# Kernel tuning notes

Measured on AMD Instinct MI355X. Metric: run time of the kernel, lower is better.

## Reference

```python
import jax, jax.numpy as jnp
import numpy as np

B, C, Ci, T, H, W = 8, 1024, 512, 8, 16, 16
BN_EPS = 1e-5


def setup_inputs() -> dict:
    key = jax.random.key(0)
    ks = jax.random.split(key, 13)
    s = 1.0 / np.sqrt(C)
    si = 1.0 / np.sqrt(Ci)
    return {
        "x": jax.random.normal(ks[0], (B, C, T, H, W), jnp.float32),
        "g_w": jax.random.normal(ks[1], (Ci, C), jnp.float32) * s,
        "g_b": jax.random.normal(ks[2], (Ci,), jnp.float32) * 0.01,
        "theta_w": jax.random.normal(ks[3], (Ci, C), jnp.float32) * s,
        "theta_b": jax.random.normal(ks[4], (Ci,), jnp.float32) * 0.01,
        "phi_w": jax.random.normal(ks[5], (Ci, C), jnp.float32) * s,
        "phi_b": jax.random.normal(ks[6], (Ci,), jnp.float32) * 0.01,
        "W_w": jax.random.normal(ks[7], (C, Ci), jnp.float32) * si,
        "W_b": jax.random.normal(ks[8], (C,), jnp.float32) * 0.01,
        "bn_gamma": jax.random.normal(ks[9], (C,), jnp.float32),
        "bn_beta": jax.random.normal(ks[10], (C,), jnp.float32) * 0.1,
        "bn_mean": jax.random.normal(ks[11], (C,), jnp.float32) * 0.1,
        "bn_var": jax.random.uniform(ks[12], (C,), jnp.float32) + 0.5,
    }


def reference(x, g_w, g_b, theta_w, theta_b, phi_w, phi_b, W_w, W_b,
              bn_gamma, bn_beta, bn_mean, bn_var):
    b = x.shape[0]
    xf = x.reshape(b, x.shape[1], -1)  # (B, C, N), N = T*H*W

    def proj(w, bias):  # 1x1 conv over flattened spatial dims == channel GEMM
        return jnp.einsum('oc,bcn->bon', w, xf) + bias[None, :, None]

    g_x = proj(g_w, g_b).transpose(0, 2, 1)          # (B, N, Ci)
    theta_x = proj(theta_w, theta_b).transpose(0, 2, 1)  # (B, N, Ci)
    phi_x = proj(phi_w, phi_b)                        # (B, Ci, N)

    f = jnp.einsum('bnc,bcm->bnm', theta_x, phi_x)    # (B, N, N) full scores
    f_div_C = jax.nn.softmax(f, axis=-1)
    y = jnp.einsum('bnm,bmc->bnc', f_div_C, g_x)      # (B, N, Ci)
    y = y.transpose(0, 2, 1)                          # (B, Ci, N)

    W_y = jnp.einsum('oc,bcn->bon', W_w, y) + W_b[None, :, None]
    # BatchNorm (inference mode with running stats)
    inv = jax.lax.rsqrt(bn_var + BN_EPS)
    W_y = (W_y - bn_mean[None, :, None]) * (inv * bn_gamma)[None, :, None] + bn_beta[None, :, None]

    z = W_y + xf
    return z.reshape(x.shape)
```

## Files before the change

kernel.cpp:

```cpp
#include <hip/hip_runtime.h>


#define B_  8
#define C_  1024
#define CI_ 512
#define N_  2048

typedef _Float16 half_t;
typedef __attribute__((ext_vector_type(8))) _Float16 f16x8;
typedef __attribute__((ext_vector_type(4))) _Float16 f16x4;
typedef __attribute__((ext_vector_type(4))) float     f32x4;

__device__ __forceinline__ void gload16(const void* g, void* l) {
  __builtin_amdgcn_global_load_lds(
      (__attribute__((address_space(1))) unsigned int*)(g),
      (__attribute__((address_space(3))) unsigned int*)(l),
      16, 0, 0);
}

__device__ __forceinline__ void gemm128(const half_t* Ag, long lda,
                                        const half_t* Bg, long ldb,
                                        int K,
                                        half_t* lA, half_t* lB,
                                        f32x4 acc[4][4])
{
  const int tid  = threadIdx.x;
  const int lane = tid & 63;
  const int wid  = tid >> 6;
  const int wm   = wid >> 1, wn = wid & 1;
  const int frow = lane & 15;
  const int g4   = lane >> 4;

  for (int k0 = 0; k0 < K; k0 += 64) {
#pragma unroll
    for (int it = 0; it < 4; ++it) {
      int c = it * 256 + tid;
      int row = c >> 3, slot = (c & 7) ^ (row & 7);
      gload16(Ag + (long)row * lda + (k0 + slot * 8), (char*)lA + c * 16);
    }
#pragma unroll
    for (int it = 0; it < 4; ++it) {
      int c = it * 256 + tid;
      int row = c >> 3, slot = (c & 7) ^ (row & 7);
      gload16(Bg + (long)row * ldb + (k0 + slot * 8), (char*)lB + c * 16);
    }
    __syncthreads();
#pragma unroll
    for (int kk = 0; kk < 2; ++kk) {
      f16x8 af[4], bfr[4];
#pragma unroll
      for (int i = 0; i < 4; ++i) {
        int row  = wm * 64 + i * 16 + frow;
        int slot = (kk * 4 + g4) ^ (row & 7);
        af[i] = *(const f16x8*)(lA + row * 64 + slot * 8);
      }
#pragma unroll
      for (int j = 0; j < 4; ++j) {
        int row  = wn * 64 + j * 16 + frow;
        int slot = (kk * 4 + g4) ^ (row & 7);
        bfr[j] = *(const f16x8*)(lB + row * 64 + slot * 8);
      }
#pragma unroll
      for (int i = 0; i < 4; ++i)
#pragma unroll
        for (int j = 0; j < 4; ++j)
          acc[i][j] = __builtin_amdgcn_mfma_f32_16x16x32_f16(af[i], bfr[j], acc[i][j], 0, 0, 0);
    }
    __syncthreads();
  }
}

__device__ __forceinline__ void zero_acc(f32x4 acc[4][4]) {
  f32x4 z = {0.f, 0.f, 0.f, 0.f};
#pragma unroll
  for (int i = 0; i < 4; ++i)
#pragma unroll
    for (int j = 0; j < 4; ++j) acc[i][j] = z;
}

__device__ __forceinline__ void dump_acc(float* ep, const f32x4 acc[4][4],
                                         int wm, int wn, int lane, int pass,
                                         const float* bias_row)
{
  if (wm != pass) return;
  int r4 = (lane >> 4) * 4, cc = lane & 15;
#pragma unroll
  for (int i = 0; i < 4; ++i) {
#pragma unroll
    for (int r = 0; r < 4; ++r) {
      int row = i * 16 + r4 + r;
      float bv = bias_row ? bias_row[row] : 0.0f;
#pragma unroll
      for (int j = 0; j < 4; ++j)
        ep[row * 128 + wn * 64 + j * 16 + cc] = acc[i][j][r] + bv;
    }
  }
}

__global__ __launch_bounds__(256) void k_prep(
    const float* theta_w, const float* phi_w, const float* g_w,
    const float* W_w, const float* W_b,
    const float* gamma, const float* beta, const float* mean, const float* var,
    half_t* Wcat, half_t* Wfin, float* bnA, float* bnB)
{
  const int PW = CI_ * C_;
  int idx = blockIdx.x * 256 + threadIdx.x;
  if (idx < PW)               Wcat[idx] = (half_t)theta_w[idx];
  else if (idx < 2 * PW)      Wcat[idx] = (half_t)phi_w[idx - PW];
  else if (idx < 3 * PW)      Wcat[idx] = (half_t)g_w[idx - 2 * PW];
  else if (idx < 4 * PW)      Wfin[idx - 3 * PW] = (half_t)W_w[idx - 3 * PW];
  else if (idx < 4 * PW + C_) {
    int o = idx - 4 * PW;
    float sc = gamma[o] * rsqrtf(var[o] + 1e-5f);
    bnA[o] = sc;
    bnB[o] = (W_b[o] - mean[o]) * sc + beta[o];
  }
}

__global__ __launch_bounds__(256) void k_transpose(const float* x, half_t* xT)
{
  __shared__ float t[32][33];
  int b = blockIdx.z, c0 = blockIdx.y * 32, n0 = blockIdx.x * 32;
  int tx = threadIdx.x, ty = threadIdx.y;
  const float* xp = x + ((long)b * C_ + c0) * N_ + n0;
#pragma unroll
  for (int j = 0; j < 4; ++j)
    t[ty + j * 8][tx] = xp[(long)(ty + j * 8) * N_ + tx];
  __syncthreads();
  half_t* xo = xT + ((long)b * N_ + n0) * C_ + c0;
#pragma unroll
  for (int j = 0; j < 4; ++j)
    xo[(long)(ty + j * 8) * C_ + tx] = (half_t)t[tx][ty + j * 8];
}

__global__ __launch_bounds__(256) void k_proj(
    const half_t* Wcat, const half_t* xT,
    const float* theta_b, const float* phi_b, const float* g_b,
    half_t* thetaT, half_t* phiT, half_t* gmat)
{
  __shared__ __align__(16) char smem[32768];
  half_t* lA = (half_t*)smem;
  half_t* lB = (half_t*)(smem + 16384);
  float*  ep = (float*)smem;

  int b = blockIdx.z, m0 = blockIdx.y * 128, n0 = blockIdx.x * 128;
  f32x4 acc[4][4];
  zero_acc(acc);
  gemm128(Wcat + (long)m0 * C_, C_, xT + ((long)b * N_ + n0) * C_, C_, C_, lA, lB, acc);

  int lane = threadIdx.x & 63, wid = threadIdx.x >> 6;
  int wm = wid >> 1, wn = wid & 1;
  int t = threadIdx.x;

  const float* bias = (m0 < 512) ? theta_b : (m0 < 1024) ? phi_b : g_b;
  int m0sub = (m0 < 512) ? m0 : (m0 < 1024) ? m0 - 512 : m0 - 1024;

#pragma unroll
  for (int pass = 0; pass < 2; ++pass) {
    __syncthreads();
    dump_acc(ep, acc, wm, wn, lane, pass, bias + m0sub + pass * 64);
    __syncthreads();
    if (m0 < 1024) {
      half_t* basep = (m0 < 512) ? thetaT : phiT;
      int ncol = t >> 1, ob = (t & 1) * 32;
      half_t* dst = basep + ((long)b * N_ + n0 + ncol) * CI_
                          + (m0sub + pass * 64 + ob);
#pragma unroll
      for (int k2 = 0; k2 < 4; ++k2) {
        f16x8 w;
#pragma unroll
        for (int e = 0; e < 8; ++e)
          w[e] = (half_t)ep[(ob + k2 * 8 + e) * 128 + ncol];
        *(f16x8*)(dst + k2 * 8) = w;
      }
    } else {
#pragma unroll
      for (int k = 0; k < 8; ++k) {
        int lin = t * 4 + k * 1024;
        int row = lin >> 7, col = lin & 127;
        int o = m0sub + pass * 64 + row;
        f32x4 v = *(const f32x4*)(ep + lin);
        f16x4 w = { (half_t)v[0], (half_t)v[1], (half_t)v[2], (half_t)v[3] };
        *(f16x4*)(gmat + ((long)b * CI_ + o) * N_ + n0 + col) = w;
      }
    }
  }
}

__global__ __launch_bounds__(256) void k_qk(
    const half_t* thetaT, const half_t* phiT, float* fbuf, int c0, int rows)
{
  __shared__ __align__(16) char smem[32768];
  half_t* lA = (half_t*)smem;
  half_t* lB = (half_t*)(smem + 16384);
  float*  ep = (float*)smem;

  int b = blockIdx.z, m0 = blockIdx.y * 128, n0 = blockIdx.x * 128;
  f32x4 acc[4][4];
  zero_acc(acc);
  gemm128(thetaT + ((long)b * N_ + c0 + m0) * CI_, CI_,
          phiT   + ((long)b * N_ + n0) * CI_,      CI_, CI_, lA, lB, acc);

  int lane = threadIdx.x & 63, wid = threadIdx.x >> 6;
  int wm = wid >> 1, wn = wid & 1;
  int t = threadIdx.x;
#pragma unroll
  for (int pass = 0; pass < 2; ++pass) {
    __syncthreads();
    dump_acc(ep, acc, wm, wn, lane, pass, nullptr);
    __syncthreads();
#pragma unroll
    for (int k = 0; k < 8; ++k) {
      int lin = t * 4 + k * 1024;
      int row = lin >> 7, col = lin & 127;
      int mr = m0 + pass * 64 + row;
      *(f32x4*)(fbuf + ((long)b * rows + mr) * N_ + n0 + col) =
          *(const f32x4*)(ep + lin);
    }
  }
}

__global__ __launch_bounds__(256) void k_softmax(float* fbuf)
{
  long row = blockIdx.x;
  float* rp = fbuf + row * N_;
  int t = threadIdx.x, lane = t & 63, wid = t >> 6;
  f32x4 a = *(const f32x4*)(rp + t * 8);
  f32x4 c = *(const f32x4*)(rp + t * 8 + 4);
  float m = fmaxf(fmaxf(fmaxf(a[0], a[1]), fmaxf(a[2], a[3])),
                  fmaxf(fmaxf(c[0], c[1]), fmaxf(c[2], c[3])));
#pragma unroll
  for (int o = 1; o < 64; o <<= 1) m = fmaxf(m, __shfl_xor(m, o));
  __shared__ float red[8];
  if (lane == 0) red[wid] = m;
  __syncthreads();
  m = fmaxf(fmaxf(red[0], red[1]), fmaxf(red[2], red[3]));
  float e[8];
  e[0] = __expf(a[0] - m); e[1] = __expf(a[1] - m);
  e[2] = __expf(a[2] - m); e[3] = __expf(a[3] - m);
  e[4] = __expf(c[0] - m); e[5] = __expf(c[1] - m);
  e[6] = __expf(c[2] - m); e[7] = __expf(c[3] - m);
  float s = ((e[0] + e[1]) + (e[2] + e[3])) + ((e[4] + e[5]) + (e[6] + e[7]));
#pragma unroll
  for (int o = 1; o < 64; o <<= 1) s += __shfl_xor(s, o);
  if (lane == 0) red[4 + wid] = s;
  __syncthreads();
  s = (red[4] + red[5]) + (red[6] + red[7]);
  float inv = 1.0f / s;
  f16x8 ph;
#pragma unroll
  for (int k = 0; k < 8; ++k) ph[k] = (half_t)(e[k] * inv);
  *(f16x8*)((half_t*)rp + t * 8) = ph;
}

__global__ __launch_bounds__(256) void k_pv(
    const half_t* P, const half_t* gmat, half_t* ybuf, int c0, int rows)
{
  __shared__ __align__(16) char smem[32768];
  half_t* lA = (half_t*)smem;
  half_t* lB = (half_t*)(smem + 16384);
  float*  ep = (float*)smem;

  int b = blockIdx.z, m0 = blockIdx.y * 128, n0 = blockIdx.x * 128;
  f32x4 acc[4][4];
  zero_acc(acc);
  gemm128(P + ((long)b * rows + m0) * (N_ * 2), N_ * 2,
          gmat + ((long)b * CI_ + n0) * N_,     N_, N_, lA, lB, acc);

  int lane = threadIdx.x & 63, wid = threadIdx.x >> 6;
  int wm = wid >> 1, wn = wid & 1;
  int t = threadIdx.x;
#pragma unroll
  for (int pass = 0; pass < 2; ++pass) {
    __syncthreads();
    dump_acc(ep, acc, wm, wn, lane, pass, nullptr);
    __syncthreads();
#pragma unroll
    for (int k = 0; k < 8; ++k) {
      int lin = t * 4 + k * 1024;
      int row = lin >> 7, col = lin & 127;
      int nr = c0 + m0 + pass * 64 + row;
      f32x4 v = *(const f32x4*)(ep + lin);
      f16x4 w = { (half_t)v[0], (half_t)v[1], (half_t)v[2], (half_t)v[3] };
      *(f16x4*)(ybuf + ((long)b * N_ + nr) * CI_ + n0 + col) = w;
    }
  }
}

__global__ __launch_bounds__(256) void k_final(
    const half_t* Wfin, const half_t* ybuf,
    const float* bnA, const float* bnB, const float* x, float* out)
{
  __shared__ __align__(16) char smem[32768];
  half_t* lA = (half_t*)smem;
  half_t* lB = (half_t*)(smem + 16384);
  float*  ep = (float*)smem;

  int b = blockIdx.z, m0 = blockIdx.y * 128, n0 = blockIdx.x * 128;
  f32x4 acc[4][4];
  zero_acc(acc);
  gemm128(Wfin + (long)m0 * CI_, CI_,
          ybuf + ((long)b * N_ + n0) * CI_, CI_, CI_, lA, lB, acc);

  int lane = threadIdx.x & 63, wid = threadIdx.x >> 6;
  int wm = wid >> 1, wn = wid & 1;
  int t = threadIdx.x;
#pragma unroll
  for (int pass = 0; pass < 2; ++pass) {
    __syncthreads();
    dump_acc(ep, acc, wm, wn, lane, pass, nullptr);
    __syncthreads();
#pragma unroll
    for (int k = 0; k < 8; ++k) {
      int lin = t * 4 + k * 1024;
      int row = lin >> 7, col = lin & 127;
      int o = m0 + pass * 64 + row;
      long idx = ((long)b * C_ + o) * N_ + n0 + col;
      f32x4 v  = *(const f32x4*)(ep + lin);
      f32x4 xi = *(const f32x4*)(x + idx);
      float sA = bnA[o], sB = bnB[o];
      f32x4 w = { v[0] * sA + sB + xi[0], v[1] * sA + sB + xi[1],
                  v[2] * sA + sB + xi[2], v[3] * sA + sB + xi[3] };
      *(f32x4*)(out + idx) = w;
    }
  }
}

extern "C" void kernel_launch(void* const* d_in, const int* in_sizes, int n_in,
                              void* d_out, int out_size, void* d_ws, size_t ws_size,
                              hipStream_t stream)
{
  const float* x       = (const float*)d_in[0];
  const float* g_w     = (const float*)d_in[1];
  const float* g_b     = (const float*)d_in[2];
  const float* theta_w = (const float*)d_in[3];
  const float* theta_b = (const float*)d_in[4];
  const float* phi_w   = (const float*)d_in[5];
  const float* phi_b   = (const float*)d_in[6];
  const float* W_w     = (const float*)d_in[7];
  const float* W_b     = (const float*)d_in[8];
  const float* gamma   = (const float*)d_in[9];
  const float* beta    = (const float*)d_in[10];
  const float* mean    = (const float*)d_in[11];
  const float* var     = (const float*)d_in[12];
  float* out = (float*)d_out;

  char* p = (char*)d_ws;
  auto alloc = [&](size_t bytes) {
    char* r = p; p += (bytes + 255) & ~(size_t)255; return r;
  };
  half_t* xT     = (half_t*)alloc((size_t)B_ * N_ * C_ * 2);
  half_t* Wcat   = (half_t*)alloc((size_t)1536 * C_ * 2);
  half_t* Wfin   = (half_t*)alloc((size_t)C_ * CI_ * 2);
  half_t* thetaT = (half_t*)alloc((size_t)B_ * N_ * CI_ * 2);
  half_t* phiT   = (half_t*)alloc((size_t)B_ * N_ * CI_ * 2);
  half_t* gmat   = (half_t*)alloc((size_t)B_ * CI_ * N_ * 2);
  half_t* ybuf   = (half_t*)alloc((size_t)B_ * N_ * CI_ * 2);
  float*  bnA    = (float*)alloc(C_ * 4);
  float*  bnB    = (float*)alloc(C_ * 4);
  size_t fixed = (size_t)(p - (char*)d_ws);

  int rows;
  if      (fixed + (size_t)B_ * 2048 * N_ * 4 <= ws_size) rows = 2048;
  else if (fixed + (size_t)B_ * 1024 * N_ * 4 <= ws_size) rows = 1024;
  else if (fixed + (size_t)B_ *  512 * N_ * 4 <= ws_size) rows = 512;
  else if (fixed + (size_t)B_ *  256 * N_ * 4 <= ws_size) rows = 256;
  else rows = 128;
  float* fbuf = (float*)alloc((size_t)B_ * rows * N_ * 4);

  k_prep<<<dim3((4 * CI_ * C_ + C_) / 256 + 1), 256, 0, stream>>>(
      theta_w, phi_w, g_w, W_w, W_b, gamma, beta, mean, var, Wcat, Wfin, bnA, bnB);
  k_transpose<<<dim3(N_ / 32, C_ / 32, B_), dim3(32, 8), 0, stream>>>(x, xT);
  k_proj<<<dim3(N_ / 128, 1536 / 128, B_), 256, 0, stream>>>(
      Wcat, xT, theta_b, phi_b, g_b, thetaT, phiT, gmat);
  for (int c0 = 0; c0 < N_; c0 += rows) {
    k_qk<<<dim3(N_ / 128, rows / 128, B_), 256, 0, stream>>>(thetaT, phiT, fbuf, c0, rows);
    k_softmax<<<dim3(B_ * rows), 256, 0, stream>>>(fbuf);
    k_pv<<<dim3(CI_ / 128, rows / 128, B_), 256, 0, stream>>>(
        (const half_t*)fbuf, gmat, ybuf, c0, rows);
  }
  k_final<<<dim3(N_ / 128, C_ / 128, B_), 256, 0, stream>>>(Wfin, ybuf, bnA, bnB, x, out);
}
```

Before: 416.9 us.

## Double-buffer LDS tiles in shared GEMM to overlap loads with MFMA

The shared 128x128 GEMM routine now keeps two LDS stages and issues the global-to-LDS loads for the next K tile before running the MFMAs on the current one. This removes one barrier per iteration and is meant to hide global load latency behind compute. Every GEMM kernel doubles its shared memory to 64 KB, which may lower the number of resident blocks per CU. The global_load_lds writes are asynchronous and only one barrier per iteration guards the buffer swap, so ordering relies on that barrier draining the outstanding loads.

Measured after the change: 388.7 us. 1.07x faster.

```diff
diff --git a/kernel.cpp b/kernel.cpp
--- a/kernel.cpp
+++ b/kernel.cpp
@@ -21,7 +21,7 @@
 __device__ __forceinline__ void gemm128(const half_t* Ag, long lda,
                                         const half_t* Bg, long ldb,
                                         int K,
-                                        half_t* lA, half_t* lB,
+                                        half_t* lds,
                                         f32x4 acc[4][4])
 {
   const int tid  = threadIdx.x;
@@ -31,7 +31,9 @@
   const int frow = lane & 15;
   const int g4   = lane >> 4;
 
-  for (int k0 = 0; k0 < K; k0 += 64) {
+  auto stage = [&](int p, int k0) {
+    half_t* lA = lds + p * 16384;
+    half_t* lB = lA + 8192;
 #pragma unroll
     for (int it = 0; it < 4; ++it) {
       int c = it * 256 + tid;
@@ -44,7 +46,15 @@
       int row = c >> 3, slot = (c & 7) ^ (row & 7);
       gload16(Bg + (long)row * ldb + (k0 + slot * 8), (char*)lB + c * 16);
     }
-    __syncthreads();
+  };
+
+  stage(0, 0);
+  __syncthreads();
+  int cur = 0;
+  for (int k0 = 64; k0 <= K; k0 += 64) {
+    if (k0 < K) stage(cur ^ 1, k0);
+    half_t* lA = lds + cur * 16384;
+    half_t* lB = lA + 8192;
 #pragma unroll
     for (int kk = 0; kk < 2; ++kk) {
       f16x8 af[4], bfr[4];
@@ -67,6 +77,7 @@
           acc[i][j] = __builtin_amdgcn_mfma_f32_16x16x32_f16(af[i], bfr[j], acc[i][j], 0, 0, 0);
     }
     __syncthreads();
+    cur ^= 1;
   }
 }
 
@@ -138,15 +149,14 @@
     const float* theta_b, const float* phi_b, const float* g_b,
     half_t* thetaT, half_t* phiT, half_t* gmat)
 {
-  __shared__ __align__(16) char smem[32768];
-  half_t* lA = (half_t*)smem;
-  half_t* lB = (half_t*)(smem + 16384);
-  float*  ep = (float*)smem;
+  __shared__ __align__(16) char smem[65536];
+  half_t* lds = (half_t*)smem;
+  float*  ep  = (float*)smem;
 
   int b = blockIdx.z, m0 = blockIdx.y * 128, n0 = blockIdx.x * 128;
   f32x4 acc[4][4];
   zero_acc(acc);
-  gemm128(Wcat + (long)m0 * C_, C_, xT + ((long)b * N_ + n0) * C_, C_, C_, lA, lB, acc);
+  gemm128(Wcat + (long)m0 * C_, C_, xT + ((long)b * N_ + n0) * C_, C_, C_, lds, acc);
 
   int lane = threadIdx.x & 63, wid = threadIdx.x >> 6;
   int wm = wid >> 1, wn = wid & 1;
@@ -190,16 +200,15 @@
 __global__ __launch_bounds__(256) void k_qk(
     const half_t* thetaT, const half_t* phiT, float* fbuf, int c0, int rows)
 {
-  __shared__ __align__(16) char smem[32768];
-  half_t* lA = (half_t*)smem;
-  half_t* lB = (half_t*)(smem + 16384);
-  float*  ep = (float*)smem;
+  __shared__ __align__(16) char smem[65536];
+  half_t* lds = (half_t*)smem;
+  float*  ep  = (float*)smem;
 
   int b = blockIdx.z, m0 = blockIdx.y * 128, n0 = blockIdx.x * 128;
   f32x4 acc[4][4];
   zero_acc(acc);
   gemm128(thetaT + ((long)b * N_ + c0 + m0) * CI_, CI_,
-          phiT   + ((long)b * N_ + n0) * CI_,      CI_, CI_, lA, lB, acc);
+          phiT   + ((long)b * N_ + n0) * CI_,      CI_, CI_, lds, acc);
 
   int lane = threadIdx.x & 63, wid = threadIdx.x >> 6;
   int wm = wid >> 1, wn = wid & 1;
@@ -256,16 +265,15 @@
 __global__ __launch_bounds__(256) void k_pv(
     const half_t* P, const half_t* gmat, half_t* ybuf, int c0, int rows)
 {
-  __shared__ __align__(16) char smem[32768];
-  half_t* lA = (half_t*)smem;
-  half_t* lB = (half_t*)(smem + 16384);
-  float*  ep = (float*)smem;
+  __shared__ __align__(16) char smem[65536];
+  half_t* lds = (half_t*)smem;
+  float*  ep  = (float*)smem;
 
   int b = blockIdx.z, m0 = blockIdx.y * 128, n0 = blockIdx.x * 128;
   f32x4 acc[4][4];
   zero_acc(acc);
   gemm128(P + ((long)b * rows + m0) * (N_ * 2), N_ * 2,
-          gmat + ((long)b * CI_ + n0) * N_,     N_, N_, lA, lB, acc);
+          gmat + ((long)b * CI_ + n0) * N_,     N_, N_, lds, acc);
 
   int lane = threadIdx.x & 63, wid = threadIdx.x >> 6;
   int wm = wid >> 1, wn = wid & 1;
@@ -291,16 +299,15 @@
     const half_t* Wfin, const half_t* ybuf,
     const float* bnA, const float* bnB, const float* x, float* out)
 {
-  __shared__ __align__(16) char smem[32768];
-  half_t* lA = (half_t*)smem;
-  half_t* lB = (half_t*)(smem + 16384);
-  float*  ep = (float*)smem;
+  __shared__ __align__(16) char smem[65536];
+  half_t* lds = (half_t*)smem;
+  float*  ep  = (float*)smem;
 
   int b = blockIdx.z, m0 = blockIdx.y * 128, n0 = blockIdx.x * 128;
   f32x4 acc[4][4];
   zero_acc(acc);
   gemm128(Wfin + (long)m0 * CI_, CI_,
-          ybuf + ((long)b * N_ + n0) * CI_, CI_, CI_, lA, lB, acc);
+          ybuf + ((long)b * N_ + n0) * CI_, CI_, CI_, lds, acc);
 
   int lane = threadIdx.x & 63, wid = threadIdx.x >> 6;
   int wm = wid >> 1, wn = wid & 1;
```
